# Optimization experiments

Hardware: AMD Instinct MI355X
Metric: run time of the kernel (lower is better)

Reference implementation:

```python
import jax, jax.numpy as jnp
import numpy as np

D_MODEL = 512
N_HEADS = 8
D_FF = 2048

def _linear_params(key, d_in, d_out):
    kw, kb = jax.random.split(key)
    bound = 1.0 / np.sqrt(d_in)
    W = jax.random.uniform(kw, (d_in, d_out), minval=-bound, maxval=bound, dtype=jnp.float32)
    b = jax.random.uniform(kb, (d_out,), minval=-bound, maxval=bound, dtype=jnp.float32)
    return W, b

def setup_inputs() -> dict:
    key = jax.random.key(0)
    ks = jax.random.split(key, 7)
    x = jax.random.normal(ks[0], (4, 2048, D_MODEL), dtype=jnp.float32)
    Wq, bq = _linear_params(ks[1], D_MODEL, D_MODEL)
    Wk, bk = _linear_params(ks[2], D_MODEL, D_MODEL)
    Wv, bv = _linear_params(ks[3], D_MODEL, D_MODEL)
    W1, b1 = _linear_params(ks[4], D_MODEL, D_FF)
    W2, b2 = _linear_params(ks[5], D_FF, D_MODEL)
    g1 = jnp.ones((D_MODEL,), jnp.float32); be1 = jnp.zeros((D_MODEL,), jnp.float32)
    g2 = jnp.ones((D_MODEL,), jnp.float32); be2 = jnp.zeros((D_MODEL,), jnp.float32)
    return {"x": x, "Wq": Wq, "bq": bq, "Wk": Wk, "bk": bk, "Wv": Wv, "bv": bv,
            "W1": W1, "b1": b1, "W2": W2, "b2": b2,
            "g1": g1, "be1": be1, "g2": g2, "be2": be2}

def _layernorm(x, g, b, eps=1e-5):
    mu = jnp.mean(x, axis=-1, keepdims=True)
    var = jnp.mean(jnp.square(x - mu), axis=-1, keepdims=True)
    return (x - mu) * jax.lax.rsqrt(var + eps) * g + b

def reference(x, Wq, bq, Wk, bk, Wv, bv, W1, b1, W2, b2, g1, be1, g2, be2):
    B, S, D = x.shape
    H = N_HEADS
    Dh = D // H
    residual = x
    xn = _layernorm(x, g1, be1)
    # [B,S,D] -> [B,H,S,Dh]
    q = (xn @ Wq + bq).reshape(B, S, H, Dh).transpose(0, 2, 1, 3)
    k = (xn @ Wk + bk).reshape(B, S, H, Dh).transpose(0, 2, 1, 3)
    v = (xn @ Wv + bv).reshape(B, S, H, Dh).transpose(0, 2, 1, 3)
    # sigmoid pointwise attention, scaled by sqrt(d_model) (not head dim)
    scores = jnp.einsum('bhsd,bhtd->bhst', q, k) / jnp.sqrt(jnp.float32(D))
    attn = jax.nn.sigmoid(scores)
    out = jnp.einsum('bhst,bhtd->bhsd', attn, v)
    out = out.transpose(0, 2, 1, 3).reshape(B, S, D)
    x = residual + out  # dropout=0 (eval)
    residual = x
    xn = _layernorm(x, g2, be2)
    ffn = jax.nn.relu(xn @ W1 + b1) @ W2 + b2
    return residual + ffn
```

## Files before the change

kernel.cpp:

```cpp
#include <hip/hip_runtime.h>
#include <hip/hip_bf16.h>
#include <math.h>

#define D_MODEL 512
#define N_HEADS 8
#define D_HEAD 64
#define D_FF 2048
#define SEQ 2048
#define BATCH 4
#define NTOK (BATCH * SEQ)
#define QSCALE 0.04419417382415922f
#define QSCALE_L2E (-QSCALE * 1.44269504089f)

typedef unsigned short ushort_t;
typedef __attribute__((ext_vector_type(8))) short short8;
typedef __attribute__((ext_vector_type(4))) float float4v;

static __device__ __forceinline__ ushort_t f2bf(float f) {
    union { float f; unsigned int i; } c; c.f = f;
    unsigned int i = c.i;
    unsigned int r = (i + 0x7FFFu + ((i >> 16) & 1u)) >> 16;
    return (ushort_t)r;
}

static __device__ __forceinline__ unsigned int pack2bf(float a, float b) {
    union { __hip_bfloat162 h; unsigned int u; } c;
    c.h = __float22bfloat162_rn(make_float2(a, b));
    return c.u;
}

static __device__ __forceinline__ float sig2(float x) {
    return __builtin_amdgcn_rcpf(1.0f + __builtin_amdgcn_exp2f(x));
}

__global__ __launch_bounds__(256) void k_prep_weights(const float* __restrict__ Wq,
                                                      const float* __restrict__ Wk,
                                                      const float* __restrict__ Wv,
                                                      const float* __restrict__ W1,
                                                      const float* __restrict__ W2,
                                                      ushort_t* __restrict__ Wqkvt,
                                                      ushort_t* __restrict__ W1t,
                                                      ushort_t* __restrict__ W2t) {
    int id = blockIdx.x * 256 + threadIdx.x;
    if (id < 3 * 262144) {
        int m = id >> 18, r = id & 262143;
        int k = r >> 9, n = r & 511;
        const float* src = (m == 0) ? Wq : ((m == 1) ? Wk : Wv);
        Wqkvt[((size_t)m * 512 + n) * 512 + k] = f2bf(src[r]);
        return;
    }
    int id2 = id - 3 * 262144;
    if (id2 < 1048576) {
        int k = id2 >> 11, n = id2 & 2047;
        W1t[(size_t)n * 512 + k] = f2bf(W1[id2]);
        return;
    }
    int id3 = id2 - 1048576;
    if (id3 < 1048576) {
        int k = id3 >> 9, n = id3 & 511;
        W2t[(size_t)n * 2048 + k] = f2bf(W2[id3]);
    }
}

__global__ __launch_bounds__(256) void k_layernorm(const float* __restrict__ X,
                                                   const float* __restrict__ g,
                                                   const float* __restrict__ be,
                                                   ushort_t* __restrict__ Out) {
    int row  = blockIdx.x * 4 + (threadIdx.x >> 6);
    int lane = threadIdx.x & 63;
    const float* x = X + (size_t)row * D_MODEL + lane * 8;
    float4 v0 = ((const float4*)x)[0];
    float4 v1 = ((const float4*)x)[1];
    float vals[8] = {v0.x, v0.y, v0.z, v0.w, v1.x, v1.y, v1.z, v1.w};
    float s = 0.f, sq = 0.f;
#pragma unroll
    for (int j = 0; j < 8; j++) { s += vals[j]; sq += vals[j] * vals[j]; }
#pragma unroll
    for (int off = 32; off; off >>= 1) { s += __shfl_xor(s, off); sq += __shfl_xor(sq, off); }
    float mu  = s * (1.0f / D_MODEL);
    float var = sq * (1.0f / D_MODEL) - mu * mu;
    float inv = rsqrtf(var + 1e-5f);
    const float* gp  = g  + lane * 8;
    const float* bp  = be + lane * 8;
    float4 g0 = ((const float4*)gp)[0], g1v = ((const float4*)gp)[1];
    float4 b0 = ((const float4*)bp)[0], b1v = ((const float4*)bp)[1];
    float gs[8] = {g0.x, g0.y, g0.z, g0.w, g1v.x, g1v.y, g1v.z, g1v.w};
    float bs[8] = {b0.x, b0.y, b0.z, b0.w, b1v.x, b1v.y, b1v.z, b1v.w};
    ushort_t o[8];
#pragma unroll
    for (int j = 0; j < 8; j++) o[j] = f2bf((vals[j] - mu) * inv * gs[j] + bs[j]);
    ushort_t* op = Out + (size_t)row * D_MODEL + lane * 8;
    *(uint4*)op = *(uint4*)o;
}

static __device__ __forceinline__ void stage_tile(const ushort_t* __restrict__ G, int K,
                                                  ushort_t* L, int nchunks, int koff,
                                                  int w, int l) {
#pragma unroll
    for (int n = w; n < nchunks; n += 4) {
        const ushort_t* g = G + (size_t)(n * 16 + (l >> 2)) * K + koff + (l & 3) * 8;
        __builtin_amdgcn_global_load_lds((const __attribute__((address_space(1))) void*)g,
                                         (__attribute__((address_space(3))) void*)(L + n * 512),
                                         16, 0, 0);
    }
}

template <int JW>
static __device__ __forceinline__ void gemm_core2(const ushort_t* __restrict__ A,
                                                  const ushort_t* __restrict__ Bt,
                                                  int K, int m0, int n0,
                                                  ushort_t* As, ushort_t* Bs,
                                                  float4v acc[4][JW]) {
    const int BBUF = JW * 1024;
    int t = threadIdx.x, w = t >> 6, l = t & 63, q = l >> 4, lm = l & 15;
    int mb = (w & 1) * 64, nb = (w >> 1) * (JW * 16);
    const ushort_t* Ab = A + (size_t)m0 * K;
    const ushort_t* Bb = Bt + (size_t)n0 * K;
    int T = K >> 5;

    stage_tile(Ab, K, As, 8, 0, w, l);
    stage_tile(Bb, K, Bs, 2 * JW, 0, w, l);
    __syncthreads();

    for (int kt = 0; kt < T; kt++) {
        int cur = kt & 1;
        if (kt + 1 < T) {
            stage_tile(Ab, K, As + (1 - cur) * 4096, 8, (kt + 1) * 32, w, l);
            stage_tile(Bb, K, Bs + (1 - cur) * BBUF, 2 * JW, (kt + 1) * 32, w, l);
        }
        const ushort_t* asb = As + cur * 4096;
        const ushort_t* bsb = Bs + cur * BBUF;
        short8 a[4], b[JW];
#pragma unroll
        for (int i = 0; i < 4; i++) a[i] = *(const short8*)&asb[(mb + 16 * i + lm) * 32 + q * 8];
#pragma unroll
        for (int j = 0; j < JW; j++) b[j] = *(const short8*)&bsb[(nb + 16 * j + lm) * 32 + q * 8];
#pragma unroll
        for (int i = 0; i < 4; i++)
#pragma unroll
            for (int j = 0; j < JW; j++)
                acc[i][j] = __builtin_amdgcn_mfma_f32_16x16x32_bf16(a[i], b[j], acc[i][j], 0, 0, 0);
        __syncthreads();
    }
}

__global__ __launch_bounds__(256) void k_gemm_qkv(const ushort_t* __restrict__ A,
                                                  const ushort_t* __restrict__ Bt,
                                                  const float* __restrict__ bq,
                                                  const float* __restrict__ bk,
                                                  const float* __restrict__ bv,
                                                  ushort_t* __restrict__ qb,
                                                  ushort_t* __restrict__ kb,
                                                  ushort_t* __restrict__ vt) {
    __shared__ __align__(16) ushort_t As[8192];
    __shared__ __align__(16) ushort_t Bs[8192];
    int m0 = blockIdx.x * 128, n0 = blockIdx.y * 128;
    float4v acc[4][4];
#pragma unroll
    for (int i = 0; i < 4; i++)
#pragma unroll
        for (int j = 0; j < 4; j++) acc[i][j] = (float4v){0.f, 0.f, 0.f, 0.f};
    gemm_core2<4>(A, Bt, D_MODEL, m0, n0, As, Bs, acc);

    int t = threadIdx.x, w = t >> 6, l = t & 63, q = l >> 4, lm = l & 15;
    int mb = (w & 1) * 64, nb = (w >> 1) * 64;
    int mat = n0 >> 9, c0 = n0 & 511;
    const float* bias = (mat == 0) ? bq : ((mat == 1) ? bk : bv);
#pragma unroll
    for (int j = 0; j < 4; j++) {
        int cl = c0 + nb + 16 * j + lm;
        int hh = cl >> 6, dh = cl & 63;
        float bvv = bias[cl];
#pragma unroll
        for (int i = 0; i < 4; i++) {
            int mr0 = m0 + mb + 16 * i + q * 4;
            int bb = mr0 >> 11, ss0 = mr0 & (SEQ - 1);
            if (mat == 2) {
                union { ushort_t s[4]; uint2 v; } pk;
#pragma unroll
                for (int r = 0; r < 4; r++) pk.s[r] = f2bf(acc[i][j][r] + bvv);
                *(uint2*)&vt[((size_t)(bb * N_HEADS + hh) * D_HEAD + dh) * SEQ + ss0] = pk.v;
            } else {
                ushort_t* dst = (mat == 0) ? qb : kb;
                float sc = (mat == 0) ? QSCALE_L2E : 1.0f;
#pragma unroll
                for (int r = 0; r < 4; r++)
                    dst[((size_t)(bb * N_HEADS + hh) * SEQ + ss0 + r) * D_HEAD + dh] =
                        f2bf((acc[i][j][r] + bvv) * sc);
            }
        }
    }
}

__global__ __launch_bounds__(256) void k_gemm_ffn1(const ushort_t* __restrict__ A,
                                                   const ushort_t* __restrict__ Bt,
                                                   const float* __restrict__ b1,
                                                   ushort_t* __restrict__ hb) {
    __shared__ __align__(16) ushort_t As[8192];
    __shared__ __align__(16) ushort_t Bs[8192];
    int m0 = blockIdx.x * 128, n0 = blockIdx.y * 128;
    float4v acc[4][4];
#pragma unroll
    for (int i = 0; i < 4; i++)
#pragma unroll
        for (int j = 0; j < 4; j++) acc[i][j] = (float4v){0.f, 0.f, 0.f, 0.f};
    gemm_core2<4>(A, Bt, D_MODEL, m0, n0, As, Bs, acc);

    int t = threadIdx.x, w = t >> 6, l = t & 63, q = l >> 4, lm = l & 15;
    int mb = (w & 1) * 64, nb = (w >> 1) * 64;
#pragma unroll
    for (int j = 0; j < 4; j++) {
        int cl = n0 + nb + 16 * j + lm;
        float bvv = b1[cl];
#pragma unroll
        for (int i = 0; i < 4; i++) {
            int mr0 = m0 + mb + 16 * i + q * 4;
#pragma unroll
            for (int r = 0; r < 4; r++)
                hb[(size_t)(mr0 + r) * D_FF + cl] = f2bf(fmaxf(acc[i][j][r] + bvv, 0.f));
        }
    }
}

__global__ __launch_bounds__(256) void k_gemm_ffn2(const ushort_t* __restrict__ A,
                                                   const ushort_t* __restrict__ Bt,
                                                   const float* __restrict__ b2,
                                                   const float* __restrict__ res,
                                                   float* __restrict__ out) {
    __shared__ __align__(16) ushort_t As[8192];
    __shared__ __align__(16) ushort_t Bs[4096];
    int m0 = blockIdx.x * 128, n0 = blockIdx.y * 64;
    float4v acc[4][2];
#pragma unroll
    for (int i = 0; i < 4; i++)
#pragma unroll
        for (int j = 0; j < 2; j++) acc[i][j] = (float4v){0.f, 0.f, 0.f, 0.f};
    gemm_core2<2>(A, Bt, D_FF, m0, n0, As, Bs, acc);

    int t = threadIdx.x, w = t >> 6, l = t & 63, q = l >> 4, lm = l & 15;
    int mb = (w & 1) * 64, nb = (w >> 1) * 32;
#pragma unroll
    for (int j = 0; j < 2; j++) {
        int cl = n0 + nb + 16 * j + lm;
        float bvv = b2[cl];
#pragma unroll
        for (int i = 0; i < 4; i++) {
            int mr0 = m0 + mb + 16 * i + q * 4;
#pragma unroll
            for (int r = 0; r < 4; r++) {
                size_t idx = (size_t)(mr0 + r) * D_MODEL + cl;
                out[idx] = acc[i][j][r] + bvv + res[idx];
            }
        }
    }
}

__global__ __launch_bounds__(512) void k_attention(const ushort_t* __restrict__ Q,
                                                   const ushort_t* __restrict__ Kb,
                                                   const ushort_t* __restrict__ Vt,
                                                   const float* __restrict__ X,
                                                   float* __restrict__ Y) {
    __shared__ ushort_t Ks[2][64][72];
    __shared__ ushort_t Vs[2][64][72];
    __shared__ ushort_t Ps[128][72];
    int bh = blockIdx.y;
    int b = bh >> 3, h = bh & 7;
    size_t base = (size_t)bh * SEQ * D_HEAD;
    int s0 = blockIdx.x * 128;
    int t = threadIdx.x, w = t >> 6, l = t & 63, q = l >> 4, lm = l & 15;
    int srow = t >> 3, sc = (t & 7) * 8;

    short8 qf[2];
#pragma unroll
    for (int kc = 0; kc < 2; kc++) {
        const ushort_t* qg = Q + base + (size_t)(s0 + 16 * w + lm) * D_HEAD + kc * 32 + q * 8;
        uint4 u = *(const uint4*)qg;
        qf[kc] = *(const short8*)&u;
    }

    float4v o[4];
#pragma unroll
    for (int dj = 0; dj < 4; dj++) o[dj] = (float4v){0.f, 0.f, 0.f, 0.f};

    uint4 kr, vr;
    const ushort_t* kg0 = Kb + base + (size_t)srow * D_HEAD + sc;
    const ushort_t* vg0 = Vt + base + (size_t)srow * SEQ + sc;

    kr = *(const uint4*)(kg0); vr = *(const uint4*)(vg0);
    *(uint4*)&Ks[0][srow][sc] = kr; *(uint4*)&Vs[0][srow][sc] = vr;
    kr = *(const uint4*)(kg0 + 64 * D_HEAD); vr = *(const uint4*)(vg0 + 64);
    __syncthreads();

    for (int tt = 0; tt < SEQ / 64; tt++) {
        int cur = tt & 1;
        float4v st[4];
#pragma unroll
        for (int mt = 0; mt < 4; mt++) st[mt] = (float4v){0.f, 0.f, 0.f, 0.f};
#pragma unroll
        for (int kc = 0; kc < 2; kc++) {
#pragma unroll
            for (int mt = 0; mt < 4; mt++) {
                short8 a = *(const short8*)&Ks[cur][16 * mt + lm][kc * 32 + q * 8];
                st[mt] = __builtin_amdgcn_mfma_f32_16x16x32_bf16(a, qf[kc], st[mt], 0, 0, 0);
            }
        }
#pragma unroll
        for (int mt = 0; mt < 4; mt++) {
            float4v s4 = st[mt];
            uint2 pk;
            pk.x = pack2bf(sig2(s4[0]), sig2(s4[1]));
            pk.y = pack2bf(sig2(s4[2]), sig2(s4[3]));
            *(uint2*)&Ps[16 * w + lm][16 * mt + 4 * q] = pk;
        }
#pragma unroll
        for (int kc = 0; kc < 2; kc++) {
            short8 ap = *(const short8*)&Ps[16 * w + lm][kc * 32 + q * 8];
#pragma unroll
            for (int dj = 0; dj < 4; dj++) {
                short8 bv = *(const short8*)&Vs[cur][16 * dj + lm][kc * 32 + q * 8];
                o[dj] = __builtin_amdgcn_mfma_f32_16x16x32_bf16(ap, bv, o[dj], 0, 0, 0);
            }
        }
        if (tt + 1 < SEQ / 64) {
            int nxt = 1 - cur;
            *(uint4*)&Ks[nxt][srow][sc] = kr; *(uint4*)&Vs[nxt][srow][sc] = vr;
            if (tt + 2 < SEQ / 64) {
                kr = *(const uint4*)(kg0 + (size_t)(tt + 2) * 64 * D_HEAD);
                vr = *(const uint4*)(vg0 + (tt + 2) * 64);
            }
        }
        __syncthreads();
    }

#pragma unroll
    for (int dj = 0; dj < 4; dj++) {
        int d = 16 * dj + lm;
#pragma unroll
        for (int r = 0; r < 4; r++) {
            int s = s0 + 16 * w + q * 4 + r;
            size_t idx = ((size_t)(b * SEQ + s)) * D_MODEL + h * D_HEAD + d;
            Y[idx] = X[idx] + o[dj][r];
        }
    }
}

extern "C" void kernel_launch(void* const* d_in, const int* in_sizes, int n_in,
                              void* d_out, int out_size, void* d_ws, size_t ws_size,
                              hipStream_t stream) {
    const float* x   = (const float*)d_in[0];
    const float* Wq  = (const float*)d_in[1];
    const float* bq  = (const float*)d_in[2];
    const float* Wk  = (const float*)d_in[3];
    const float* bk  = (const float*)d_in[4];
    const float* Wv  = (const float*)d_in[5];
    const float* bv  = (const float*)d_in[6];
    const float* W1  = (const float*)d_in[7];
    const float* b1  = (const float*)d_in[8];
    const float* W2  = (const float*)d_in[9];
    const float* b2  = (const float*)d_in[10];
    const float* g1  = (const float*)d_in[11];
    const float* be1 = (const float*)d_in[12];
    const float* g2  = (const float*)d_in[13];
    const float* be2 = (const float*)d_in[14];
    float* out = (float*)d_out;

    char* p = (char*)d_ws;
    ushort_t* xn    = (ushort_t*)p; p += (size_t)NTOK * D_MODEL * 2;
    ushort_t* yn    = (ushort_t*)p; p += (size_t)NTOK * D_MODEL * 2;
    float*    y     = (float*)p;    p += (size_t)NTOK * D_MODEL * 4;
    ushort_t* qb    = (ushort_t*)p; p += (size_t)NTOK * D_MODEL * 2;
    ushort_t* kb    = (ushort_t*)p; p += (size_t)NTOK * D_MODEL * 2;
    ushort_t* vt    = (ushort_t*)p; p += (size_t)NTOK * D_MODEL * 2;
    ushort_t* hb    = (ushort_t*)p; p += (size_t)NTOK * D_FF * 2;
    ushort_t* Wqkvt = (ushort_t*)p; p += (size_t)3 * D_MODEL * D_MODEL * 2;
    ushort_t* W1t   = (ushort_t*)p; p += (size_t)D_MODEL * D_FF * 2;
    ushort_t* W2t   = (ushort_t*)p; p += (size_t)D_FF * D_MODEL * 2;

    k_prep_weights<<<(3 * 262144 + 2 * 1048576 + 255) / 256, 256, 0, stream>>>(
        Wq, Wk, Wv, W1, W2, Wqkvt, W1t, W2t);

    k_layernorm<<<NTOK / 4, 256, 0, stream>>>(x, g1, be1, xn);

    dim3 gq(NTOK / 128, (3 * D_MODEL) / 128);
    k_gemm_qkv<<<gq, 256, 0, stream>>>(xn, Wqkvt, bq, bk, bv, qb, kb, vt);

    dim3 ga(SEQ / 128, BATCH * N_HEADS);
    k_attention<<<ga, 512, 0, stream>>>(qb, kb, vt, x, y);

    k_layernorm<<<NTOK / 4, 256, 0, stream>>>(y, g2, be2, yn);

    dim3 g1d(NTOK / 128, D_FF / 128);
    k_gemm_ffn1<<<g1d, 256, 0, stream>>>(yn, W1t, b1, hb);
    dim3 g2d(NTOK / 128, D_MODEL / 64);
    k_gemm_ffn2<<<g2d, 256, 0, stream>>>(hb, W2t, b2, y, out);
}
```

Baseline: 257.0 us.

## Split attention key range across warps with register-held K/V and LDS reduction

The attention kernel now gives each block 64 query rows and 4 warps. Each warp handles a disjoint quarter of the key sequence and loads K and V fragments straight from global memory into registers instead of staging them through double-buffered shared memory. Partial outputs are summed in shared memory over serialized turns, and the residual add is then written with vectorized float4 stores. This removes the per-tile block-wide barriers and the LDS staging of K/V, and gives each K/V fragment more query reuse. The cost is higher register pressure, uncoalesced global fragment loads with no software prefetch, and a serialized cross-warp reduction at the end.

```diff
diff --git a/kernel.cpp b/kernel.cpp
--- a/kernel.cpp
+++ b/kernel.cpp
@@ -255,91 +255,125 @@
     }
 }
 
-__global__ __launch_bounds__(512) void k_attention(const ushort_t* __restrict__ Q,
-                                                   const ushort_t* __restrict__ Kb,
-                                                   const ushort_t* __restrict__ Vt,
-                                                   const float* __restrict__ X,
-                                                   float* __restrict__ Y) {
-    __shared__ ushort_t Ks[2][64][72];
-    __shared__ ushort_t Vs[2][64][72];
-    __shared__ ushort_t Ps[128][72];
+__global__ __launch_bounds__(256, 2) void k_attention(const ushort_t* __restrict__ Q,
+                                                      const ushort_t* __restrict__ Kb,
+                                                      const ushort_t* __restrict__ Vt,
+                                                      const float* __restrict__ X,
+                                                      float* __restrict__ Y) {
+    __shared__ __align__(16) ushort_t Ps[4 * 4096];
+    float* Osum = (float*)Ps;
+
     int bh = blockIdx.y;
     int b = bh >> 3, h = bh & 7;
     size_t base = (size_t)bh * SEQ * D_HEAD;
-    int s0 = blockIdx.x * 128;
+    int s0 = blockIdx.x * 64;
     int t = threadIdx.x, w = t >> 6, l = t & 63, q = l >> 4, lm = l & 15;
-    int srow = t >> 3, sc = (t & 7) * 8;
-
-    short8 qf[2];
-#pragma unroll
-    for (int kc = 0; kc < 2; kc++) {
-        const ushort_t* qg = Q + base + (size_t)(s0 + 16 * w + lm) * D_HEAD + kc * 32 + q * 8;
-        uint4 u = *(const uint4*)qg;
-        qf[kc] = *(const short8*)&u;
-    }
-
-    float4v o[4];
-#pragma unroll
-    for (int dj = 0; dj < 4; dj++) o[dj] = (float4v){0.f, 0.f, 0.f, 0.f};
-
-    uint4 kr, vr;
-    const ushort_t* kg0 = Kb + base + (size_t)srow * D_HEAD + sc;
-    const ushort_t* vg0 = Vt + base + (size_t)srow * SEQ + sc;
-
-    kr = *(const uint4*)(kg0); vr = *(const uint4*)(vg0);
-    *(uint4*)&Ks[0][srow][sc] = kr; *(uint4*)&Vs[0][srow][sc] = vr;
-    kr = *(const uint4*)(kg0 + 64 * D_HEAD); vr = *(const uint4*)(vg0 + 64);
+    int wb = w * 4096;
+    int sw3 = lm & 3;
+
+    const ushort_t* qg = Q + base + (size_t)(s0 + lm) * D_HEAD + q * 8;
+    short8 qf[4][2];
+#pragma unroll
+    for (int nt = 0; nt < 4; nt++)
+#pragma unroll
+        for (int kc = 0; kc < 2; kc++) {
+            uint4 u = *(const uint4*)(qg + nt * 16 * D_HEAD + kc * 32);
+            qf[nt][kc] = *(const short8*)&u;
+        }
+
+    float4v o[4][4];
+#pragma unroll
+    for (int sj = 0; sj < 4; sj++)
+#pragma unroll
+        for (int dj = 0; dj < 4; dj++) o[sj][dj] = (float4v){0.f, 0.f, 0.f, 0.f};
+
+    const ushort_t* kgb = Kb + base + (size_t)lm * D_HEAD + q * 8;
+    const ushort_t* vgb = Vt + base + (size_t)lm * SEQ + q * 8;
+
+    for (int ci = 0; ci < 8; ci++) {
+        int t0 = (ci * 4 + w) * 64;
+        short8 kf[4][2];
+#pragma unroll
+        for (int mt = 0; mt < 4; mt++)
+#pragma unroll
+            for (int kc = 0; kc < 2; kc++) {
+                uint4 u = *(const uint4*)(kgb + (size_t)(t0 + mt * 16) * D_HEAD + kc * 32);
+                kf[mt][kc] = *(const short8*)&u;
+            }
+        short8 vf[4][2];
+#pragma unroll
+        for (int dj = 0; dj < 4; dj++)
+#pragma unroll
+            for (int kc = 0; kc < 2; kc++) {
+                uint4 u = *(const uint4*)(vgb + (size_t)dj * 16 * SEQ + t0 + kc * 32);
+                vf[dj][kc] = *(const short8*)&u;
+            }
+#pragma unroll
+        for (int mt = 0; mt < 4; mt++) {
+            float4v st[4];
+#pragma unroll
+            for (int nt = 0; nt < 4; nt++) st[nt] = (float4v){0.f, 0.f, 0.f, 0.f};
+#pragma unroll
+            for (int kc = 0; kc < 2; kc++)
+#pragma unroll
+                for (int nt = 0; nt < 4; nt++)
+                    st[nt] = __builtin_amdgcn_mfma_f32_16x16x32_bf16(kf[mt][kc], qf[nt][kc], st[nt], 0, 0, 0);
+#pragma unroll
+            for (int nt = 0; nt < 4; nt++) {
+                uint2 pk;
+                pk.x = pack2bf(sig2(st[nt][0]), sig2(st[nt][1]));
+                pk.y = pack2bf(sig2(st[nt][2]), sig2(st[nt][3]));
+                *(uint2*)&Ps[wb + (16 * nt + lm) * 64 + ((mt ^ sw3) << 4) + 4 * q] = pk;
+            }
+        }
+#pragma unroll
+        for (int kc = 0; kc < 2; kc++) {
+#pragma unroll
+            for (int sj = 0; sj < 4; sj++) {
+                short8 ap = *(const short8*)&Ps[wb + (16 * sj + lm) * 64 +
+                                                (((2 * kc + (q >> 1)) ^ sw3) << 4) + (q & 1) * 8];
+#pragma unroll
+                for (int dj = 0; dj < 4; dj++)
+                    o[sj][dj] = __builtin_amdgcn_mfma_f32_16x16x32_bf16(ap, vf[dj][kc], o[sj][dj], 0, 0, 0);
+            }
+        }
+    }
+
     __syncthreads();
-
-    for (int tt = 0; tt < SEQ / 64; tt++) {
-        int cur = tt & 1;
-        float4v st[4];
-#pragma unroll
-        for (int mt = 0; mt < 4; mt++) st[mt] = (float4v){0.f, 0.f, 0.f, 0.f};
-#pragma unroll
-        for (int kc = 0; kc < 2; kc++) {
-#pragma unroll
-            for (int mt = 0; mt < 4; mt++) {
-                short8 a = *(const short8*)&Ks[cur][16 * mt + lm][kc * 32 + q * 8];
-                st[mt] = __builtin_amdgcn_mfma_f32_16x16x32_bf16(a, qf[kc], st[mt], 0, 0, 0);
-            }
-        }
-#pragma unroll
-        for (int mt = 0; mt < 4; mt++) {
-            float4v s4 = st[mt];
-            uint2 pk;
-            pk.x = pack2bf(sig2(s4[0]), sig2(s4[1]));
-            pk.y = pack2bf(sig2(s4[2]), sig2(s4[3]));
-            *(uint2*)&Ps[16 * w + lm][16 * mt + 4 * q] = pk;
-        }
-#pragma unroll
-        for (int kc = 0; kc < 2; kc++) {
-            short8 ap = *(const short8*)&Ps[16 * w + lm][kc * 32 + q * 8];
-#pragma unroll
-            for (int dj = 0; dj < 4; dj++) {
-                short8 bv = *(const short8*)&Vs[cur][16 * dj + lm][kc * 32 + q * 8];
-                o[dj] = __builtin_amdgcn_mfma_f32_16x16x32_bf16(ap, bv, o[dj], 0, 0, 0);
-            }
-        }
-        if (tt + 1 < SEQ / 64) {
-            int nxt = 1 - cur;
-            *(uint4*)&Ks[nxt][srow][sc] = kr; *(uint4*)&Vs[nxt][srow][sc] = vr;
-            if (tt + 2 < SEQ / 64) {
-                kr = *(const uint4*)(kg0 + (size_t)(tt + 2) * 64 * D_HEAD);
-                vr = *(const uint4*)(vg0 + (tt + 2) * 64);
-            }
+#pragma unroll 1
+    for (int turn = 0; turn < 4; turn++) {
+        if (w == turn) {
+#pragma unroll
+            for (int sj = 0; sj < 4; sj++)
+#pragma unroll
+                for (int dj = 0; dj < 4; dj++) {
+                    int d = 16 * dj + lm;
+#pragma unroll
+                    for (int r = 0; r < 4; r++) {
+                        int sl = 16 * sj + 4 * q + r;
+                        float* p = &Osum[sl * 66 + d];
+                        float v = o[sj][dj][r];
+                        *p = (turn == 0) ? v : (*p + v);
+                    }
+                }
         }
         __syncthreads();
     }
 
-#pragma unroll
-    for (int dj = 0; dj < 4; dj++) {
-        int d = 16 * dj + lm;
-#pragma unroll
-        for (int r = 0; r < 4; r++) {
-            int s = s0 + 16 * w + q * 4 + r;
-            size_t idx = ((size_t)(b * SEQ + s)) * D_MODEL + h * D_HEAD + d;
-            Y[idx] = X[idx] + o[dj][r];
+    {
+        int row = t >> 2, c0 = (t & 3) * 16;
+        size_t gro = ((size_t)(b * SEQ + s0 + row)) * D_MODEL + h * D_HEAD + c0;
+        const float* xp = X + gro;
+        float* yp = Y + gro;
+        const float* os = &Osum[row * 66 + c0];
+#pragma unroll
+        for (int i = 0; i < 4; i++) {
+            float4 xv = *(const float4*)(xp + i * 4);
+            float4 ov = *(const float4*)(os + i * 4);
+            float4 rr;
+            rr.x = xv.x + ov.x; rr.y = xv.y + ov.y;
+            rr.z = xv.z + ov.z; rr.w = xv.w + ov.w;
+            *(float4*)(yp + i * 4) = rr;
         }
     }
 }
@@ -384,8 +418,8 @@
     dim3 gq(NTOK / 128, (3 * D_MODEL) / 128);
     k_gemm_qkv<<<gq, 256, 0, stream>>>(xn, Wqkvt, bq, bk, bv, qb, kb, vt);
 
-    dim3 ga(SEQ / 128, BATCH * N_HEADS);
-    k_attention<<<ga, 512, 0, stream>>>(qb, kb, vt, x, y);
+    dim3 ga(SEQ / 64, BATCH * N_HEADS);
+    k_attention<<<ga, 256, 0, stream>>>(qb, kb, vt, x, y);
 
     k_layernorm<<<NTOK / 4, 256, 0, stream>>>(y, g2, be2, yn);
 
```

Measured after the change: 284.1 us. +10.5%, slower.
